# Kernel tuning notes

Measured on AMD Instinct MI355X. Metric: run time of the kernel, lower is better.

Reference implementation:

```python
import jax, jax.numpy as jnp
import numpy as np

BIAS_VALUE = -1e30


def apply_rope(inputs, positions, max_wavelength=10000):
    # inputs: [B, T, H, Dh]; positions: [B, T]
    head_dim = inputs.shape[-1]
    fraction = 2 * jnp.arange(0, head_dim // 2) / head_dim
    timescale = max_wavelength ** fraction
    sinusoid_inp = positions[..., jnp.newaxis] / timescale[jnp.newaxis, :]  # [B, T, Dh/2]
    sinusoid_inp = sinusoid_inp[..., jnp.newaxis, :]                        # [B, T, 1, Dh/2]
    sin = jnp.sin(sinusoid_inp)
    cos = jnp.cos(sinusoid_inp)
    first_half, second_half = jnp.split(inputs, 2, axis=-1)
    first_part = first_half * cos - second_half * sin
    second_part = second_half * cos + first_half * sin
    return jnp.concatenate([first_part, second_part], axis=-1).astype(inputs.dtype)


def rms_norm(x, scale):
    var = jnp.mean(jnp.square(x), axis=-1, keepdims=True)
    return x * jax.lax.rsqrt(var + 1e-6) * (1 + scale)


def setup_inputs() -> dict:
    key = jax.random.key(0)
    ks = jax.random.split(key, 12)
    B, T, D, H, Dh = 4, 2048, 512, 8, 64
    q = jax.random.normal(ks[0], (B, T, D), jnp.float32)
    kv = jax.random.normal(ks[1], (B, T, D), jnp.float32)
    mask = jnp.broadcast_to(jnp.tril(jnp.ones((T, T), bool))[None, None], (B, 1, T, T))
    pos = jnp.broadcast_to(jnp.arange(T, dtype=jnp.int32), (B, T))
    s = 0.02
    return {
        "q": q, "kv": kv, "mask": mask, "q_positions": pos, "kv_positions": pos,
        "wq": jax.random.normal(ks[2], (D, H * Dh), jnp.float32) * s,
        "bq": jnp.zeros((H * Dh,), jnp.float32),
        "wk": jax.random.normal(ks[3], (D, H * Dh), jnp.float32) * s,
        "bk": jnp.zeros((H * Dh,), jnp.float32),
        "wv": jax.random.normal(ks[4], (D, H * Dh), jnp.float32) * s,
        "bv": jnp.zeros((H * Dh,), jnp.float32),
        "scale_q": jax.random.normal(ks[5], (Dh,), jnp.float32) * s,
        "scale_k": jax.random.normal(ks[6], (Dh,), jnp.float32) * s,
        "wo": jax.random.normal(ks[7], (H * Dh, D), jnp.float32) * s,
        "bo": jnp.zeros((D,), jnp.float32),
    }


def reference(q, kv, mask, q_positions, kv_positions,
              wq, bq, wk, bk, wv, bv, scale_q, scale_k, wo, bo):
    B, T, D = q.shape
    H = 8
    Dh = wq.shape[1] // H
    qk_size = Dh

    def proj(x, w, b):
        y = x @ w + b
        return y.reshape(*x.shape[:-1], H, -1)  # [B, T, H, Dh]

    query_heads = rms_norm(proj(q, wq, bq), scale_q)
    key_heads = rms_norm(proj(kv, wk, bk), scale_k)
    value_heads = proj(kv, wv, bv)

    query_heads = apply_rope(query_heads, q_positions)
    key_heads = apply_rope(key_heads, kv_positions)

    attn_logits = jnp.einsum('bthd,bThd->bhtT', query_heads, key_heads)
    attn_logits = attn_logits / np.sqrt(qk_size).astype(q.dtype)
    attn_logits = jnp.where(mask, attn_logits, BIAS_VALUE)
    attn_weights = jax.nn.softmax(attn_logits, axis=-1)
    attn_weights = jnp.where(mask, attn_weights, 0)
    attn = jnp.einsum('bhtT,bThd->bthd', attn_weights, value_heads)
    attn = attn.reshape(B, T, -1)
    return attn @ wo + bo
```

## Files before the change

### kernel.cpp

```cpp
#include <hip/hip_runtime.h>
#include <hip/hip_bf16.h>
#include <cstdint>

#define B_ 4
#define T_ 2048
#define D_ 512
#define H_ 8

typedef __bf16 bf16x8 __attribute__((ext_vector_type(8)));
typedef __bf16 bf16x4 __attribute__((ext_vector_type(4)));
typedef float f32x4 __attribute__((ext_vector_type(4)));

__device__ inline void gload_lds16(const void* g, void* l) {
    __builtin_amdgcn_global_load_lds(
        (const __attribute__((address_space(1))) void*)g,
        (__attribute__((address_space(3))) void*)l, 16, 0, 0);
}

__global__ void cast2_kernel(const float* __restrict__ qf, const float* __restrict__ kvf,
                             __bf16* __restrict__ qb, __bf16* __restrict__ kvb, int n4) {
    int stride = gridDim.x * blockDim.x;
    for (int i = blockIdx.x * blockDim.x + threadIdx.x; i < 2 * n4; i += stride) {
        const float* src = (i < n4) ? qf : kvf;
        __bf16* dst = (i < n4) ? qb : kvb;
        int j = (i < n4) ? i : i - n4;
        float4 v = reinterpret_cast<const float4*>(src)[j];
        bf16x4 o = { (__bf16)v.x, (__bf16)v.y, (__bf16)v.z, (__bf16)v.w };
        reinterpret_cast<bf16x4*>(dst)[j] = o;
    }
}

__global__ void transpose_w4_kernel(const float* __restrict__ wq, const float* __restrict__ wk,
                                    const float* __restrict__ wv, const float* __restrict__ wo,
                                    __bf16* __restrict__ wqkvT, __bf16* __restrict__ woT) {
    __shared__ float tile[32][33];
    int z = blockIdx.z;
    const float* in = (z == 0) ? wq : (z == 1) ? wk : (z == 2) ? wv : wo;
    __bf16* out = (z < 3) ? wqkvT + (size_t)z * D_ * D_ : woT;
    int tx = threadIdx.x & 31, ty = threadIdx.x >> 5;
    int r0 = blockIdx.y * 32, c0 = blockIdx.x * 32;
#pragma unroll
    for (int i = 0; i < 4; i++)
        tile[ty + i * 8][tx] = in[(size_t)(r0 + ty + i * 8) * D_ + c0 + tx];
    __syncthreads();
#pragma unroll
    for (int i = 0; i < 4; i++)
        out[(size_t)(c0 + ty + i * 8) * D_ + r0 + tx] = (__bf16)tile[tx][ty + i * 8];
}

__global__ void rope_table_kernel(float2* __restrict__ tab) {
    int i = blockIdx.x * 256 + threadIdx.x;
    int p = i >> 5, d2 = i & 31;
    float inv_ts = exp2f((float)d2 * (-13.28771237954945f / 32.0f));
    float ang = (float)p * inv_ts;
    float sv, cv;
    __sincosf(ang, &sv, &cv);
    tab[i] = make_float2(cv, sv);
}

template<int MODE>
__global__ __launch_bounds__(256, 2) void gemm_tile_kernel(
    const __bf16* __restrict__ Xq, const __bf16* __restrict__ Xkv,
    const __bf16* __restrict__ WT,
    const float* __restrict__ biasQ, const float* __restrict__ biasK,
    const float* __restrict__ biasV,
    float* __restrict__ outf, __bf16* __restrict__ qh, __bf16* __restrict__ kh,
    __bf16* __restrict__ vt,
    const float* __restrict__ scale_q, const float* __restrict__ scale_k,
    const int* __restrict__ qpos, const int* __restrict__ kpos,
    const float2* __restrict__ rtab, int M, int Ntot, int K) {
    __shared__ __bf16 Ab[2][128 * 32];
    __shared__ __bf16 Bb[2][128 * 32];

    const int tid = threadIdx.x;
    const int lane = tid & 63, widx = tid >> 6;
    const int lo = lane & 15, hi = lane >> 4;
    const int wm = widx >> 1, wn = widx & 1;

    const int nwg = gridDim.x;
    const int q8 = nwg >> 3;
    int bid = blockIdx.x;
    int swz = (bid & 7) * q8 + (bid >> 3);
    const int ntn = Ntot >> 7;
    const int m0 = (swz / ntn) << 7;
    const int nt = swz % ntn;
    const int n0g = nt << 7;
    const int seg = (MODE == 3) ? (nt >> 2) : 0;
    const __bf16* X = (MODE == 3 && seg > 0) ? Xkv : Xq;

    const int srow = tid >> 2;
    const int sslot = tid & 3;

    f32x4 acc[4][4] = {};

    auto stage = [&](int kc, int bufi) {
#pragma unroll
        for (int i = 0; i < 2; i++) {
            int row = i * 64 + srow;
            int cs = sslot ^ ((row >> 1) & 3);
            gload_lds16(X + (size_t)(m0 + row) * K + kc + cs * 8,
                        &Ab[bufi][(i * 64 + widx * 16) * 32]);
        }
#pragma unroll
        for (int i = 0; i < 2; i++) {
            int row = i * 64 + srow;
            int cs = sslot ^ ((row >> 1) & 3);
            gload_lds16(WT + (size_t)(n0g + row) * K + kc + cs * 8,
                        &Bb[bufi][(i * 64 + widx * 16) * 32]);
        }
    };

    const int nks = K >> 5;
    stage(0, 0);
    __syncthreads();
    int cur = 0;

    for (int ks = 0; ks < nks; ks++) {
        if (ks + 1 < nks) stage((ks + 1) << 5, cur ^ 1);

        bf16x8 a[4], bvec[4];
#pragma unroll
        for (int mf = 0; mf < 4; mf++) {
            int R = wm * 64 + mf * 16 + lo;
            a[mf] = *reinterpret_cast<const bf16x8*>(&Ab[cur][R * 32 + ((hi ^ ((R >> 1) & 3)) << 3)]);
        }
#pragma unroll
        for (int nf = 0; nf < 4; nf++) {
            int R = wn * 64 + nf * 16 + lo;
            bvec[nf] = *reinterpret_cast<const bf16x8*>(&Bb[cur][R * 32 + ((hi ^ ((R >> 1) & 3)) << 3)]);
        }
#pragma unroll
        for (int mf = 0; mf < 4; mf++)
#pragma unroll
            for (int nf = 0; nf < 4; nf++)
                acc[mf][nf] = __builtin_amdgcn_mfma_f32_16x16x32_bf16(a[mf], bvec[nf], acc[mf][nf], 0, 0, 0);

        __syncthreads();
        cur ^= 1;
    }

    const int mrow0 = m0 + wm * 64;

    if (MODE == 0) {
        const int ncol0 = n0g + wn * 64;
        float bs[4];
#pragma unroll
        for (int nf = 0; nf < 4; nf++) bs[nf] = biasQ[ncol0 + nf * 16 + lo];
#pragma unroll
        for (int mf = 0; mf < 4; mf++)
#pragma unroll
            for (int nf = 0; nf < 4; nf++)
#pragma unroll
                for (int r = 0; r < 4; r++) {
                    int row = mrow0 + mf * 16 + hi * 4 + r;
                    outf[(size_t)row * Ntot + ncol0 + nf * 16 + lo] = acc[mf][nf][r] + bs[nf];
                }
    } else {
        const int ncol0 = ((nt & 3) << 7) + wn * 64;
        const int h = ncol0 >> 6;
        const float* bias = (seg == 0) ? biasQ : (seg == 1) ? biasK : biasV;
        float bs[4];
#pragma unroll
        for (int nf = 0; nf < 4; nf++) bs[nf] = bias[ncol0 + nf * 16 + lo];

        if (seg < 2) {
            const float* scale = seg ? scale_k : scale_q;
            const int* pos = seg ? kpos : qpos;
            __bf16* dst0 = seg ? kh : qh;
            float sc4[4];
#pragma unroll
            for (int nf = 0; nf < 4; nf++) sc4[nf] = 1.0f + scale[nf * 16 + lo];
#pragma unroll
            for (int mf = 0; mf < 4; mf++) {
#pragma unroll
                for (int r = 0; r < 4; r++) {
                    int row = mrow0 + mf * 16 + hi * 4 + r;
                    float y0 = acc[mf][0][r] + bs[0];
                    float y1 = acc[mf][1][r] + bs[1];
                    float y2 = acc[mf][2][r] + bs[2];
                    float y3 = acc[mf][3][r] + bs[3];
                    float ps = y0 * y0 + y1 * y1 + y2 * y2 + y3 * y3;
#pragma unroll
                    for (int off = 1; off < 16; off <<= 1) ps += __shfl_xor(ps, off);
                    float rmsf = rsqrtf(ps * (1.0f / 64.0f) + 1e-6f);
                    int p = pos[row];
                    float2 c0 = rtab[p * 32 + lo];
                    float2 c1 = rtab[p * 32 + 16 + lo];
                    float z0 = y0 * rmsf * sc4[0];
                    float z1 = y1 * rmsf * sc4[1];
                    float z2 = y2 * rmsf * sc4[2];
                    float z3 = y3 * rmsf * sc4[3];
                    int b = row >> 11, t = row & (T_ - 1);
                    __bf16* dst = dst0 + ((size_t)(b * H_ + h) * T_ + t) * 64;
                    dst[lo]      = (__bf16)(z0 * c0.x - z2 * c0.y);
                    dst[16 + lo] = (__bf16)(z1 * c1.x - z3 * c1.y);
                    dst[32 + lo] = (__bf16)(z2 * c0.x + z0 * c0.y);
                    dst[48 + lo] = (__bf16)(z3 * c1.x + z1 * c1.y);
                }
            }
        } else {
#pragma unroll
            for (int mf = 0; mf < 4; mf++) {
                int row0 = mrow0 + mf * 16 + hi * 4;
                int b = row0 >> 11, t0 = row0 & (T_ - 1);
#pragma unroll
                for (int nf = 0; nf < 4; nf++) {
                    int d = nf * 16 + lo;
                    bf16x4 pk = { (__bf16)(acc[mf][nf][0] + bs[nf]), (__bf16)(acc[mf][nf][1] + bs[nf]),
                                  (__bf16)(acc[mf][nf][2] + bs[nf]), (__bf16)(acc[mf][nf][3] + bs[nf]) };
                    *reinterpret_cast<bf16x4*>(vt + ((size_t)(b * H_ + h) * 64 + d) * T_ + t0) = pk;
                }
            }
        }
    }
}

__global__ __launch_bounds__(256, 3) void attn_kernel(const __bf16* __restrict__ qh,
                                                      const __bf16* __restrict__ kh,
                                                      const __bf16* __restrict__ vt,
                                                      __bf16* __restrict__ attn) {
    __shared__ __bf16 kbuf[2][64 * 64];
    __shared__ __bf16 vbuf[2][64 * 64];
    __shared__ __bf16 plds[4][16][72];

    const int lane = threadIdx.x & 63, widx = threadIdx.x >> 6;
    const int lo = lane & 15, hi = lane >> 4;
    const int bh = blockIdx.x;
    const int sid = 31 - blockIdx.y;
    const int ntiles = sid + 1;
    const int qb = sid * 64 + widx * 16;
    const __bf16* Qg = qh + (size_t)bh * T_ * 64;
    const __bf16* Kg = kh + (size_t)bh * T_ * 64;
    const __bf16* Vg = vt + (size_t)bh * 64 * T_;
    const int b = bh >> 3, h = bh & 7;

    const int srow = lane >> 3;
    const int sslot = lane & 7;
    const int schunk = sslot ^ srow;

    bf16x8 qa[2];
#pragma unroll
    for (int c = 0; c < 2; c++)
        qa[c] = *reinterpret_cast<const bf16x8*>(Qg + (size_t)(qb + lo) * 64 + c * 32 + hi * 8);

    f32x4 o[4] = {};
    float m = -1e30f, l = 0.0f;

    auto stage = [&](int tile, int bufi) {
        const int kvb0 = tile * 64;
#pragma unroll
        for (int i = 0; i < 2; i++) {
            int r = widx * 16 + i * 8 + srow;
            gload_lds16(Kg + (size_t)(kvb0 + r) * 64 + schunk * 8,
                        &kbuf[bufi][(widx * 16 + i * 8) * 64]);
        }
#pragma unroll
        for (int i = 0; i < 2; i++) {
            int r = widx * 16 + i * 8 + srow;
            gload_lds16(Vg + (size_t)r * T_ + kvb0 + schunk * 8,
                        &vbuf[bufi][(widx * 16 + i * 8) * 64]);
        }
    };

    stage(0, 0);
    __syncthreads();
    int cur = 0;

    for (int j = 0; j < ntiles; ++j) {
        if (j + 1 < ntiles) stage(j + 1, cur ^ 1);

        f32x4 s[4] = {};
        __builtin_amdgcn_s_setprio(1);
#pragma unroll
        for (int c = 0; c < 2; c++) {
#pragma unroll
            for (int f = 0; f < 4; f++) {
                int R = f * 16 + lo;
                int C = c * 4 + hi;
                bf16x8 kb = *reinterpret_cast<const bf16x8*>(
                    &kbuf[cur][R * 64 + ((C ^ (lo & 7)) << 3)]);
                s[f] = __builtin_amdgcn_mfma_f32_16x16x32_bf16(kb, qa[c], s[f], 0, 0, 0);
            }
        }
        __builtin_amdgcn_s_setprio(0);

        const bool diag = (j == ntiles - 1);
        float pm = -1e30f;
#pragma unroll
        for (int f = 0; f < 4; f++)
#pragma unroll
            for (int r = 0; r < 4; r++) {
                float v = s[f][r];
                if (diag && (f * 16 + hi * 4 + r > widx * 16 + lo)) v = -1e30f;
                s[f][r] = v;
                pm = fmaxf(pm, v);
            }
        pm = fmaxf(pm, __shfl_xor(pm, 16));
        pm = fmaxf(pm, __shfl_xor(pm, 32));

        if (!__all(pm <= m + 64.0f)) {
            float mn = fmaxf(m, pm);
            float alpha = __expf((m - mn) * 0.125f);
            l *= alpha;
#pragma unroll
            for (int n = 0; n < 4; n++)
#pragma unroll
                for (int r = 0; r < 4; r++) o[n][r] *= alpha;
            m = mn;
        }

        const float negm = -m * 0.125f;
        float ps = 0.0f;
        bf16x4 pk[4];
#pragma unroll
        for (int f = 0; f < 4; f++) {
#pragma unroll
            for (int r = 0; r < 4; r++) {
                float e = __expf(fmaf(s[f][r], 0.125f, negm));
                ps += e;
                pk[f][r] = (__bf16)e;
            }
        }
        ps += __shfl_xor(ps, 16);
        ps += __shfl_xor(ps, 32);
        l += ps;

#pragma unroll
        for (int f = 0; f < 4; f++)
            *reinterpret_cast<bf16x4*>(&plds[widx][lo][f * 16 + hi * 4]) = pk[f];
        bf16x8 pa0 = *reinterpret_cast<const bf16x8*>(&plds[widx][lo][hi * 8]);
        bf16x8 pa1 = *reinterpret_cast<const bf16x8*>(&plds[widx][lo][32 + hi * 8]);

        __builtin_amdgcn_s_setprio(1);
#pragma unroll
        for (int n = 0; n < 4; n++) {
#pragma unroll
            for (int c = 0; c < 2; c++) {
                int R = n * 16 + lo;
                int C = c * 4 + hi;
                bf16x8 vb = *reinterpret_cast<const bf16x8*>(
                    &vbuf[cur][R * 64 + ((C ^ (lo & 7)) << 3)]);
                o[n] = __builtin_amdgcn_mfma_f32_16x16x32_bf16(vb, c ? pa1 : pa0, o[n], 0, 0, 0);
            }
        }
        __builtin_amdgcn_s_setprio(0);

        __syncthreads();
        cur ^= 1;
    }

    const float inv = 1.0f / l;
    const int qrow = qb + lo;
#pragma unroll
    for (int n = 0; n < 4; n++) {
        bf16x4 pk = { (__bf16)(o[n][0] * inv), (__bf16)(o[n][1] * inv),
                      (__bf16)(o[n][2] * inv), (__bf16)(o[n][3] * inv) };
        *reinterpret_cast<bf16x4*>(attn + ((size_t)b * T_ + qrow) * D_ + h * 64 + n * 16 + hi * 4) = pk;
    }
}

extern "C" void kernel_launch(void* const* d_in, const int* in_sizes, int n_in,
                              void* d_out, int out_size, void* d_ws, size_t ws_size,
                              hipStream_t stream) {
    const float* q  = (const float*)d_in[0];
    const float* kv = (const float*)d_in[1];
    const int* qpos = (const int*)d_in[3];
    const int* kpos = (const int*)d_in[4];
    const float* wq = (const float*)d_in[5];
    const float* bq = (const float*)d_in[6];
    const float* wk = (const float*)d_in[7];
    const float* bk = (const float*)d_in[8];
    const float* wv = (const float*)d_in[9];
    const float* bv = (const float*)d_in[10];
    const float* scale_q = (const float*)d_in[11];
    const float* scale_k = (const float*)d_in[12];
    const float* wo = (const float*)d_in[13];
    const float* bo = (const float*)d_in[14];
    float* out = (float*)d_out;

    char* ws = (char*)d_ws;
    size_t off = 0;
    auto alloc = [&](size_t bytes) {
        void* p = ws + off;
        off += (bytes + 255) & ~(size_t)255;
        return p;
    };
    const size_t MD = (size_t)B_ * T_ * D_;
    __bf16* qb16   = (__bf16*)alloc(MD * 2);
    __bf16* kvb16  = (__bf16*)alloc(MD * 2);
    __bf16* wqkvT  = (__bf16*)alloc((size_t)3 * D_ * D_ * 2);
    __bf16* woT    = (__bf16*)alloc((size_t)D_ * D_ * 2);
    __bf16* qh  = (__bf16*)alloc(MD * 2);
    __bf16* kh  = (__bf16*)alloc(MD * 2);
    __bf16* vt  = (__bf16*)alloc(MD * 2);
    float2* rtab = (float2*)alloc((size_t)T_ * 32 * sizeof(float2));
    __bf16* attn = qb16;

    cast2_kernel<<<2048, 256, 0, stream>>>(q, kv, qb16, kvb16, (int)(MD / 4));
    transpose_w4_kernel<<<dim3(16, 16, 4), 256, 0, stream>>>(wq, wk, wv, wo, wqkvT, woT);
    rope_table_kernel<<<(T_ * 32) / 256, 256, 0, stream>>>(rtab);

    const int M = B_ * T_;
    gemm_tile_kernel<3><<<(M / 128) * (3 * D_ / 128), 256, 0, stream>>>(
        qb16, kvb16, wqkvT, bq, bk, bv, nullptr, qh, kh, vt,
        scale_q, scale_k, qpos, kpos, rtab, M, 3 * D_, D_);
    attn_kernel<<<dim3(B_ * H_, 32), 256, 0, stream>>>(qh, kh, vt, attn);
    gemm_tile_kernel<0><<<(M / 128) * (D_ / 128), 256, 0, stream>>>(
        attn, nullptr, woT, bo, nullptr, nullptr, out, nullptr, nullptr, nullptr,
        nullptr, nullptr, nullptr, nullptr, nullptr, M, D_, D_);
}
```

Measured before the change: 96.53 us.

## Double attention query tile per block and fold softmax scale into Q

Each attention block now processes 128 query rows (32 per warp, two 16-row groups) instead of 64, so each staged K/V tile feeds twice as many MFMAs and the grid halves. The softmax scale 1/sqrt(64)*log2(e) is folded into the Q projection epilogue, so the attention loop can use exp2f directly without a per-element multiply. The lazy-rescale threshold is adjusted to match the log2 domain. This raises register use per warp and halves the block count. It also leaves some warps idle on the final diagonal tile, which may reduce occupancy and load balance.

```diff
diff --git a/kernel.cpp b/kernel.cpp
--- a/kernel.cpp
+++ b/kernel.cpp
@@ -10,6 +10,9 @@
 typedef __bf16 bf16x8 __attribute__((ext_vector_type(8)));
 typedef __bf16 bf16x4 __attribute__((ext_vector_type(4)));
 typedef float f32x4 __attribute__((ext_vector_type(4)));
+
+#define QSCALE 0.18033688011112042f
+#define DEFER_THR 11.5415603f
 
 __device__ inline void gload_lds16(const void* g, void* l) {
     __builtin_amdgcn_global_load_lds(
@@ -167,9 +170,10 @@
             const float* scale = seg ? scale_k : scale_q;
             const int* pos = seg ? kpos : qpos;
             __bf16* dst0 = seg ? kh : qh;
+            const float qmul = seg ? 1.0f : QSCALE;
             float sc4[4];
 #pragma unroll
-            for (int nf = 0; nf < 4; nf++) sc4[nf] = 1.0f + scale[nf * 16 + lo];
+            for (int nf = 0; nf < 4; nf++) sc4[nf] = (1.0f + scale[nf * 16 + lo]) * qmul;
 #pragma unroll
             for (int mf = 0; mf < 4; mf++) {
 #pragma unroll
@@ -221,14 +225,14 @@
                                                       __bf16* __restrict__ attn) {
     __shared__ __bf16 kbuf[2][64 * 64];
     __shared__ __bf16 vbuf[2][64 * 64];
-    __shared__ __bf16 plds[4][16][72];
+    __shared__ __bf16 plds[4][32][72];
 
     const int lane = threadIdx.x & 63, widx = threadIdx.x >> 6;
     const int lo = lane & 15, hi = lane >> 4;
     const int bh = blockIdx.x;
-    const int sid = 31 - blockIdx.y;
-    const int ntiles = sid + 1;
-    const int qb = sid * 64 + widx * 16;
+    const int sid = 15 - blockIdx.y;
+    const int ntiles = 2 * sid + 2;
+    const int qb = sid * 128 + widx * 32;
     const __bf16* Qg = qh + (size_t)bh * T_ * 64;
     const __bf16* Kg = kh + (size_t)bh * T_ * 64;
     const __bf16* Vg = vt + (size_t)bh * 64 * T_;
@@ -238,13 +242,16 @@
     const int sslot = lane & 7;
     const int schunk = sslot ^ srow;
 
-    bf16x8 qa[2];
-#pragma unroll
-    for (int c = 0; c < 2; c++)
-        qa[c] = *reinterpret_cast<const bf16x8*>(Qg + (size_t)(qb + lo) * 64 + c * 32 + hi * 8);
-
-    f32x4 o[4] = {};
-    float m = -1e30f, l = 0.0f;
+    bf16x8 qa[2][2];
+#pragma unroll
+    for (int g = 0; g < 2; g++)
+#pragma unroll
+        for (int c = 0; c < 2; c++)
+            qa[g][c] = *reinterpret_cast<const bf16x8*>(
+                Qg + (size_t)(qb + g * 16 + lo) * 64 + c * 32 + hi * 8);
+
+    f32x4 o[2][4] = {};
+    float m[2] = { -1e30f, -1e30f }, l[2] = { 0.0f, 0.0f };
 
     auto stage = [&](int tile, int bufi) {
         const int kvb0 = tile * 64;
@@ -269,93 +276,118 @@
     for (int j = 0; j < ntiles; ++j) {
         if (j + 1 < ntiles) stage(j + 1, cur ^ 1);
 
-        f32x4 s[4] = {};
-        __builtin_amdgcn_s_setprio(1);
-#pragma unroll
-        for (int c = 0; c < 2; c++) {
-#pragma unroll
-            for (int f = 0; f < 4; f++) {
-                int R = f * 16 + lo;
-                int C = c * 4 + hi;
-                bf16x8 kb = *reinterpret_cast<const bf16x8*>(
-                    &kbuf[cur][R * 64 + ((C ^ (lo & 7)) << 3)]);
-                s[f] = __builtin_amdgcn_mfma_f32_16x16x32_bf16(kb, qa[c], s[f], 0, 0, 0);
-            }
-        }
-        __builtin_amdgcn_s_setprio(0);
-
-        const bool diag = (j == ntiles - 1);
-        float pm = -1e30f;
-#pragma unroll
-        for (int f = 0; f < 4; f++)
-#pragma unroll
-            for (int r = 0; r < 4; r++) {
-                float v = s[f][r];
-                if (diag && (f * 16 + hi * 4 + r > widx * 16 + lo)) v = -1e30f;
-                s[f][r] = v;
-                pm = fmaxf(pm, v);
-            }
-        pm = fmaxf(pm, __shfl_xor(pm, 16));
-        pm = fmaxf(pm, __shfl_xor(pm, 32));
-
-        if (!__all(pm <= m + 64.0f)) {
-            float mn = fmaxf(m, pm);
-            float alpha = __expf((m - mn) * 0.125f);
-            l *= alpha;
-#pragma unroll
-            for (int n = 0; n < 4; n++)
-#pragma unroll
-                for (int r = 0; r < 4; r++) o[n][r] *= alpha;
-            m = mn;
-        }
-
-        const float negm = -m * 0.125f;
-        float ps = 0.0f;
-        bf16x4 pk[4];
-#pragma unroll
-        for (int f = 0; f < 4; f++) {
-#pragma unroll
-            for (int r = 0; r < 4; r++) {
-                float e = __expf(fmaf(s[f][r], 0.125f, negm));
-                ps += e;
-                pk[f][r] = (__bf16)e;
-            }
-        }
-        ps += __shfl_xor(ps, 16);
-        ps += __shfl_xor(ps, 32);
-        l += ps;
-
-#pragma unroll
-        for (int f = 0; f < 4; f++)
-            *reinterpret_cast<bf16x4*>(&plds[widx][lo][f * 16 + hi * 4]) = pk[f];
-        bf16x8 pa0 = *reinterpret_cast<const bf16x8*>(&plds[widx][lo][hi * 8]);
-        bf16x8 pa1 = *reinterpret_cast<const bf16x8*>(&plds[widx][lo][32 + hi * 8]);
-
-        __builtin_amdgcn_s_setprio(1);
-#pragma unroll
-        for (int n = 0; n < 4; n++) {
+        const int dj = j - 2 * sid;
+        const bool active = !(dj == 1 && widx < 2);
+        if (active) {
+            f32x4 s[2][4] = {};
+            __builtin_amdgcn_s_setprio(1);
 #pragma unroll
             for (int c = 0; c < 2; c++) {
-                int R = n * 16 + lo;
-                int C = c * 4 + hi;
-                bf16x8 vb = *reinterpret_cast<const bf16x8*>(
-                    &vbuf[cur][R * 64 + ((C ^ (lo & 7)) << 3)]);
-                o[n] = __builtin_amdgcn_mfma_f32_16x16x32_bf16(vb, c ? pa1 : pa0, o[n], 0, 0, 0);
-            }
-        }
-        __builtin_amdgcn_s_setprio(0);
+#pragma unroll
+                for (int f = 0; f < 4; f++) {
+                    int R = f * 16 + lo;
+                    int C = c * 4 + hi;
+                    bf16x8 kb = *reinterpret_cast<const bf16x8*>(
+                        &kbuf[cur][R * 64 + ((C ^ (lo & 7)) << 3)]);
+                    s[0][f] = __builtin_amdgcn_mfma_f32_16x16x32_bf16(kb, qa[0][c], s[0][f], 0, 0, 0);
+                    s[1][f] = __builtin_amdgcn_mfma_f32_16x16x32_bf16(kb, qa[1][c], s[1][f], 0, 0, 0);
+                }
+            }
+            __builtin_amdgcn_s_setprio(0);
+
+            const bool diag = (dj == 0 && widx < 2) || (dj == 1 && widx >= 2);
+            float pm[2] = { -1e30f, -1e30f };
+#pragma unroll
+            for (int g = 0; g < 2; g++)
+#pragma unroll
+                for (int f = 0; f < 4; f++)
+#pragma unroll
+                    for (int r = 0; r < 4; r++) {
+                        float v = s[g][f][r];
+                        if (diag && (j * 64 + f * 16 + hi * 4 + r > qb + g * 16 + lo)) v = -1e30f;
+                        s[g][f][r] = v;
+                        pm[g] = fmaxf(pm[g], v);
+                    }
+#pragma unroll
+            for (int g = 0; g < 2; g++) {
+                pm[g] = fmaxf(pm[g], __shfl_xor(pm[g], 16));
+                pm[g] = fmaxf(pm[g], __shfl_xor(pm[g], 32));
+            }
+
+            if (!__all(fmaxf(pm[0] - m[0], pm[1] - m[1]) <= DEFER_THR)) {
+#pragma unroll
+                for (int g = 0; g < 2; g++) {
+                    float mn = fmaxf(m[g], pm[g]);
+                    float alpha = exp2f(m[g] - mn);
+                    l[g] *= alpha;
+#pragma unroll
+                    for (int n = 0; n < 4; n++)
+#pragma unroll
+                        for (int r = 0; r < 4; r++) o[g][n][r] *= alpha;
+                    m[g] = mn;
+                }
+            }
+
+            bf16x4 pk[2][4];
+#pragma unroll
+            for (int g = 0; g < 2; g++) {
+                float ps = 0.0f;
+#pragma unroll
+                for (int f = 0; f < 4; f++)
+#pragma unroll
+                    for (int r = 0; r < 4; r++) {
+                        float e = exp2f(s[g][f][r] - m[g]);
+                        ps += e;
+                        pk[g][f][r] = (__bf16)e;
+                    }
+                ps += __shfl_xor(ps, 16);
+                ps += __shfl_xor(ps, 32);
+                l[g] += ps;
+            }
+
+#pragma unroll
+            for (int g = 0; g < 2; g++)
+#pragma unroll
+                for (int f = 0; f < 4; f++)
+                    *reinterpret_cast<bf16x4*>(&plds[widx][g * 16 + lo][f * 16 + hi * 4]) = pk[g][f];
+            bf16x8 pa[2][2];
+#pragma unroll
+            for (int g = 0; g < 2; g++)
+#pragma unroll
+                for (int c = 0; c < 2; c++)
+                    pa[g][c] = *reinterpret_cast<const bf16x8*>(
+                        &plds[widx][g * 16 + lo][c * 32 + hi * 8]);
+
+            __builtin_amdgcn_s_setprio(1);
+#pragma unroll
+            for (int n = 0; n < 4; n++) {
+#pragma unroll
+                for (int c = 0; c < 2; c++) {
+                    int R = n * 16 + lo;
+                    int C = c * 4 + hi;
+                    bf16x8 vb = *reinterpret_cast<const bf16x8*>(
+                        &vbuf[cur][R * 64 + ((C ^ (lo & 7)) << 3)]);
+                    o[0][n] = __builtin_amdgcn_mfma_f32_16x16x32_bf16(vb, pa[0][c], o[0][n], 0, 0, 0);
+                    o[1][n] = __builtin_amdgcn_mfma_f32_16x16x32_bf16(vb, pa[1][c], o[1][n], 0, 0, 0);
+                }
+            }
+            __builtin_amdgcn_s_setprio(0);
+        }
 
         __syncthreads();
         cur ^= 1;
     }
 
-    const float inv = 1.0f / l;
-    const int qrow = qb + lo;
-#pragma unroll
-    for (int n = 0; n < 4; n++) {
-        bf16x4 pk = { (__bf16)(o[n][0] * inv), (__bf16)(o[n][1] * inv),
-                      (__bf16)(o[n][2] * inv), (__bf16)(o[n][3] * inv) };
-        *reinterpret_cast<bf16x4*>(attn + ((size_t)b * T_ + qrow) * D_ + h * 64 + n * 16 + hi * 4) = pk;
+#pragma unroll
+    for (int g = 0; g < 2; g++) {
+        const float inv = 1.0f / l[g];
+        const int qrow = qb + g * 16 + lo;
+#pragma unroll
+        for (int n = 0; n < 4; n++) {
+            bf16x4 pk = { (__bf16)(o[g][n][0] * inv), (__bf16)(o[g][n][1] * inv),
+                          (__bf16)(o[g][n][2] * inv), (__bf16)(o[g][n][3] * inv) };
+            *reinterpret_cast<bf16x4*>(attn + ((size_t)b * T_ + qrow) * D_ + h * 64 + n * 16 + hi * 4) = pk;
+        }
     }
 }
 
@@ -404,7 +436,7 @@
     gemm_tile_kernel<3><<<(M / 128) * (3 * D_ / 128), 256, 0, stream>>>(
         qb16, kvb16, wqkvT, bq, bk, bv, nullptr, qh, kh, vt,
         scale_q, scale_k, qpos, kpos, rtab, M, 3 * D_, D_);
-    attn_kernel<<<dim3(B_ * H_, 32), 256, 0, stream>>>(qh, kh, vt, attn);
+    attn_kernel<<<dim3(B_ * H_, 16), 256, 0, stream>>>(qh, kh, vt, attn);
     gemm_tile_kernel<0><<<(M / 128) * (D_ / 128), 256, 0, stream>>>(
         attn, nullptr, woT, bo, nullptr, nullptr, out, nullptr, nullptr, nullptr,
         nullptr, nullptr, nullptr, nullptr, nullptr, M, D_, D_);
```

New measurement: 122.7 us. +27.1%, slower.

## Use 128-row query blocks with 8 waves and fold softmax scale into Q

Applied to the files above, without the earlier changes.

The attention kernel now processes 128 query rows per block with 512 threads (8 waves), so each K/V tile staged in LDS is shared by twice as many query rows and each thread issues one load per tile instead of two. The last tile is skipped by the first four waves, whose rows are fully masked there. The 1/sqrt(d)*log2(e) factor is folded into the Q projection epilogue so the softmax uses exp2 without a per-element multiply, and the deferred-rescale threshold is adjusted to match. Costs are fewer blocks (less parallelism and coarser causal load balance), some idle waves on the diagonal tile, and Q rounded to bf16 after scaling.

```diff
diff --git a/kernel.cpp b/kernel.cpp
--- a/kernel.cpp
+++ b/kernel.cpp
@@ -10,6 +10,9 @@
 typedef __bf16 bf16x8 __attribute__((ext_vector_type(8)));
 typedef __bf16 bf16x4 __attribute__((ext_vector_type(4)));
 typedef float f32x4 __attribute__((ext_vector_type(4)));
+
+#define QSCALE 0.18033688011112042f
+#define DEFER_THR 11.5415603f
 
 __device__ inline void gload_lds16(const void* g, void* l) {
     __builtin_amdgcn_global_load_lds(
@@ -167,9 +170,10 @@
             const float* scale = seg ? scale_k : scale_q;
             const int* pos = seg ? kpos : qpos;
             __bf16* dst0 = seg ? kh : qh;
+            const float qmul = seg ? 1.0f : QSCALE;
             float sc4[4];
 #pragma unroll
-            for (int nf = 0; nf < 4; nf++) sc4[nf] = 1.0f + scale[nf * 16 + lo];
+            for (int nf = 0; nf < 4; nf++) sc4[nf] = (1.0f + scale[nf * 16 + lo]) * qmul;
 #pragma unroll
             for (int mf = 0; mf < 4; mf++) {
 #pragma unroll
@@ -215,28 +219,27 @@
     }
 }
 
-__global__ __launch_bounds__(256, 3) void attn_kernel(const __bf16* __restrict__ qh,
+__global__ __launch_bounds__(512, 6) void attn_kernel(const __bf16* __restrict__ qh,
                                                       const __bf16* __restrict__ kh,
                                                       const __bf16* __restrict__ vt,
                                                       __bf16* __restrict__ attn) {
     __shared__ __bf16 kbuf[2][64 * 64];
     __shared__ __bf16 vbuf[2][64 * 64];
-    __shared__ __bf16 plds[4][16][72];
+    __shared__ __bf16 plds[8][16][72];
 
     const int lane = threadIdx.x & 63, widx = threadIdx.x >> 6;
     const int lo = lane & 15, hi = lane >> 4;
     const int bh = blockIdx.x;
-    const int sid = 31 - blockIdx.y;
-    const int ntiles = sid + 1;
-    const int qb = sid * 64 + widx * 16;
+    const int sid = 15 - blockIdx.y;
+    const int ntiles = 2 * sid + 2;
+    const int qb = sid * 128 + widx * 16;
     const __bf16* Qg = qh + (size_t)bh * T_ * 64;
     const __bf16* Kg = kh + (size_t)bh * T_ * 64;
     const __bf16* Vg = vt + (size_t)bh * 64 * T_;
     const int b = bh >> 3, h = bh & 7;
 
-    const int srow = lane >> 3;
-    const int sslot = lane & 7;
-    const int schunk = sslot ^ srow;
+    const int srow = widx * 8 + (lane >> 3);
+    const int schunk = (lane & 7) ^ (srow & 7);
 
     bf16x8 qa[2];
 #pragma unroll
@@ -248,18 +251,10 @@
 
     auto stage = [&](int tile, int bufi) {
         const int kvb0 = tile * 64;
-#pragma unroll
-        for (int i = 0; i < 2; i++) {
-            int r = widx * 16 + i * 8 + srow;
-            gload_lds16(Kg + (size_t)(kvb0 + r) * 64 + schunk * 8,
-                        &kbuf[bufi][(widx * 16 + i * 8) * 64]);
-        }
-#pragma unroll
-        for (int i = 0; i < 2; i++) {
-            int r = widx * 16 + i * 8 + srow;
-            gload_lds16(Vg + (size_t)r * T_ + kvb0 + schunk * 8,
-                        &vbuf[bufi][(widx * 16 + i * 8) * 64]);
-        }
+        gload_lds16(Kg + (size_t)(kvb0 + srow) * 64 + schunk * 8,
+                    &kbuf[bufi][widx * 8 * 64]);
+        gload_lds16(Vg + (size_t)srow * T_ + kvb0 + schunk * 8,
+                    &vbuf[bufi][widx * 8 * 64]);
     };
 
     stage(0, 0);
@@ -269,81 +264,84 @@
     for (int j = 0; j < ntiles; ++j) {
         if (j + 1 < ntiles) stage(j + 1, cur ^ 1);
 
-        f32x4 s[4] = {};
-        __builtin_amdgcn_s_setprio(1);
-#pragma unroll
-        for (int c = 0; c < 2; c++) {
+        const int dj = j - 2 * sid;
+        const bool active = !(dj == 1 && widx < 4);
+        if (active) {
+            f32x4 s[4] = {};
+            __builtin_amdgcn_s_setprio(1);
+#pragma unroll
+            for (int c = 0; c < 2; c++) {
+#pragma unroll
+                for (int f = 0; f < 4; f++) {
+                    int R = f * 16 + lo;
+                    int C = c * 4 + hi;
+                    bf16x8 kb = *reinterpret_cast<const bf16x8*>(
+                        &kbuf[cur][R * 64 + ((C ^ (lo & 7)) << 3)]);
+                    s[f] = __builtin_amdgcn_mfma_f32_16x16x32_bf16(kb, qa[c], s[f], 0, 0, 0);
+                }
+            }
+            __builtin_amdgcn_s_setprio(0);
+
+            const bool diag = (dj == 0 && widx < 4) || (dj == 1 && widx >= 4);
+            float pm = -1e30f;
+#pragma unroll
+            for (int f = 0; f < 4; f++)
+#pragma unroll
+                for (int r = 0; r < 4; r++) {
+                    float v = s[f][r];
+                    if (diag && (j * 64 + f * 16 + hi * 4 + r > qb + lo)) v = -1e30f;
+                    s[f][r] = v;
+                    pm = fmaxf(pm, v);
+                }
+            pm = fmaxf(pm, __shfl_xor(pm, 16));
+            pm = fmaxf(pm, __shfl_xor(pm, 32));
+
+            if (!__all(pm <= m + DEFER_THR)) {
+                float mn = fmaxf(m, pm);
+                float alpha = exp2f(m - mn);
+                l *= alpha;
+#pragma unroll
+                for (int n = 0; n < 4; n++)
+#pragma unroll
+                    for (int r = 0; r < 4; r++) o[n][r] *= alpha;
+                m = mn;
+            }
+
+            float ps = 0.0f;
+            bf16x4 pk[4];
 #pragma unroll
             for (int f = 0; f < 4; f++) {
-                int R = f * 16 + lo;
-                int C = c * 4 + hi;
-                bf16x8 kb = *reinterpret_cast<const bf16x8*>(
-                    &kbuf[cur][R * 64 + ((C ^ (lo & 7)) << 3)]);
-                s[f] = __builtin_amdgcn_mfma_f32_16x16x32_bf16(kb, qa[c], s[f], 0, 0, 0);
-            }
-        }
-        __builtin_amdgcn_s_setprio(0);
-
-        const bool diag = (j == ntiles - 1);
-        float pm = -1e30f;
-#pragma unroll
-        for (int f = 0; f < 4; f++)
-#pragma unroll
-            for (int r = 0; r < 4; r++) {
-                float v = s[f][r];
-                if (diag && (f * 16 + hi * 4 + r > widx * 16 + lo)) v = -1e30f;
-                s[f][r] = v;
-                pm = fmaxf(pm, v);
-            }
-        pm = fmaxf(pm, __shfl_xor(pm, 16));
-        pm = fmaxf(pm, __shfl_xor(pm, 32));
-
-        if (!__all(pm <= m + 64.0f)) {
-            float mn = fmaxf(m, pm);
-            float alpha = __expf((m - mn) * 0.125f);
-            l *= alpha;
-#pragma unroll
-            for (int n = 0; n < 4; n++)
-#pragma unroll
-                for (int r = 0; r < 4; r++) o[n][r] *= alpha;
-            m = mn;
-        }
-
-        const float negm = -m * 0.125f;
-        float ps = 0.0f;
-        bf16x4 pk[4];
-#pragma unroll
-        for (int f = 0; f < 4; f++) {
-#pragma unroll
-            for (int r = 0; r < 4; r++) {
-                float e = __expf(fmaf(s[f][r], 0.125f, negm));
-                ps += e;
-                pk[f][r] = (__bf16)e;
-            }
-        }
-        ps += __shfl_xor(ps, 16);
-        ps += __shfl_xor(ps, 32);
-        l += ps;
-
-#pragma unroll
-        for (int f = 0; f < 4; f++)
-            *reinterpret_cast<bf16x4*>(&plds[widx][lo][f * 16 + hi * 4]) = pk[f];
-        bf16x8 pa0 = *reinterpret_cast<const bf16x8*>(&plds[widx][lo][hi * 8]);
-        bf16x8 pa1 = *reinterpret_cast<const bf16x8*>(&plds[widx][lo][32 + hi * 8]);
-
-        __builtin_amdgcn_s_setprio(1);
-#pragma unroll
-        for (int n = 0; n < 4; n++) {
-#pragma unroll
-            for (int c = 0; c < 2; c++) {
-                int R = n * 16 + lo;
-                int C = c * 4 + hi;
-                bf16x8 vb = *reinterpret_cast<const bf16x8*>(
-                    &vbuf[cur][R * 64 + ((C ^ (lo & 7)) << 3)]);
-                o[n] = __builtin_amdgcn_mfma_f32_16x16x32_bf16(vb, c ? pa1 : pa0, o[n], 0, 0, 0);
-            }
-        }
-        __builtin_amdgcn_s_setprio(0);
+#pragma unroll
+                for (int r = 0; r < 4; r++) {
+                    float e = exp2f(s[f][r] - m);
+                    ps += e;
+                    pk[f][r] = (__bf16)e;
+                }
+            }
+            ps += __shfl_xor(ps, 16);
+            ps += __shfl_xor(ps, 32);
+            l += ps;
+
+#pragma unroll
+            for (int f = 0; f < 4; f++)
+                *reinterpret_cast<bf16x4*>(&plds[widx][lo][f * 16 + hi * 4]) = pk[f];
+            bf16x8 pa0 = *reinterpret_cast<const bf16x8*>(&plds[widx][lo][hi * 8]);
+            bf16x8 pa1 = *reinterpret_cast<const bf16x8*>(&plds[widx][lo][32 + hi * 8]);
+
+            __builtin_amdgcn_s_setprio(1);
+#pragma unroll
+            for (int n = 0; n < 4; n++) {
+#pragma unroll
+                for (int c = 0; c < 2; c++) {
+                    int R = n * 16 + lo;
+                    int C = c * 4 + hi;
+                    bf16x8 vb = *reinterpret_cast<const bf16x8*>(
+                        &vbuf[cur][R * 64 + ((C ^ (lo & 7)) << 3)]);
+                    o[n] = __builtin_amdgcn_mfma_f32_16x16x32_bf16(vb, c ? pa1 : pa0, o[n], 0, 0, 0);
+                }
+            }
+            __builtin_amdgcn_s_setprio(0);
+        }
 
         __syncthreads();
         cur ^= 1;
@@ -353,9 +351,9 @@
     const int qrow = qb + lo;
 #pragma unroll
     for (int n = 0; n < 4; n++) {
-        bf16x4 pk = { (__bf16)(o[n][0] * inv), (__bf16)(o[n][1] * inv),
-                      (__bf16)(o[n][2] * inv), (__bf16)(o[n][3] * inv) };
-        *reinterpret_cast<bf16x4*>(attn + ((size_t)b * T_ + qrow) * D_ + h * 64 + n * 16 + hi * 4) = pk;
+        bf16x4 pko = { (__bf16)(o[n][0] * inv), (__bf16)(o[n][1] * inv),
+                       (__bf16)(o[n][2] * inv), (__bf16)(o[n][3] * inv) };
+        *reinterpret_cast<bf16x4*>(attn + ((size_t)b * T_ + qrow) * D_ + h * 64 + n * 16 + hi * 4) = pko;
     }
 }
 
@@ -404,7 +402,7 @@
     gemm_tile_kernel<3><<<(M / 128) * (3 * D_ / 128), 256, 0, stream>>>(
         qb16, kvb16, wqkvT, bq, bk, bv, nullptr, qh, kh, vt,
         scale_q, scale_k, qpos, kpos, rtab, M, 3 * D_, D_);
-    attn_kernel<<<dim3(B_ * H_, 32), 256, 0, stream>>>(qh, kh, vt, attn);
+    attn_kernel<<<dim3(B_ * H_, 16), 512, 0, stream>>>(qh, kh, vt, attn);
     gemm_tile_kernel<0><<<(M / 128) * (D_ / 128), 256, 0, stream>>>(
         attn, nullptr, woT, bo, nullptr, nullptr, out, nullptr, nullptr, nullptr,
         nullptr, nullptr, nullptr, nullptr, nullptr, M, D_, D_);
```

Measured after the change: 110.4 us. 1.14x slower.

## Fold softmax scale into Q and use fixed max shift instead of online max

Applied to the files above, without the earlier changes.

The 1/sqrt(d)·log2(e) factor is folded into the Q RMS-norm scale in the projection epilogue. The attention loop then drops the running-max computation, its cross-lane shuffles and the rescaling of the output accumulators. A constant shift of -16 is preloaded into the MFMA accumulator so each logit becomes a single exp2. This relies on QK-norm bounding the logits, so it risks overflow or underflow if scale_q or scale_k were large.

```diff
diff --git a/kernel.cpp b/kernel.cpp
--- a/kernel.cpp
+++ b/kernel.cpp
@@ -10,6 +10,9 @@
 typedef __bf16 bf16x8 __attribute__((ext_vector_type(8)));
 typedef __bf16 bf16x4 __attribute__((ext_vector_type(4)));
 typedef float f32x4 __attribute__((ext_vector_type(4)));
+
+#define QSCALE 0.18033688011112042f
+#define MSHIFT 16.0f
 
 __device__ inline void gload_lds16(const void* g, void* l) {
     __builtin_amdgcn_global_load_lds(
@@ -167,9 +170,10 @@
             const float* scale = seg ? scale_k : scale_q;
             const int* pos = seg ? kpos : qpos;
             __bf16* dst0 = seg ? kh : qh;
+            const float qmul = seg ? 1.0f : QSCALE;
             float sc4[4];
 #pragma unroll
-            for (int nf = 0; nf < 4; nf++) sc4[nf] = 1.0f + scale[nf * 16 + lo];
+            for (int nf = 0; nf < 4; nf++) sc4[nf] = (1.0f + scale[nf * 16 + lo]) * qmul;
 #pragma unroll
             for (int mf = 0; mf < 4; mf++) {
 #pragma unroll
@@ -244,7 +248,8 @@
         qa[c] = *reinterpret_cast<const bf16x8*>(Qg + (size_t)(qb + lo) * 64 + c * 32 + hi * 8);
 
     f32x4 o[4] = {};
-    float m = -1e30f, l = 0.0f;
+    float l = 0.0f;
+    const f32x4 minit = { -MSHIFT, -MSHIFT, -MSHIFT, -MSHIFT };
 
     auto stage = [&](int tile, int bufi) {
         const int kvb0 = tile * 64;
@@ -269,7 +274,7 @@
     for (int j = 0; j < ntiles; ++j) {
         if (j + 1 < ntiles) stage(j + 1, cur ^ 1);
 
-        f32x4 s[4] = {};
+        f32x4 s[4] = { minit, minit, minit, minit };
         __builtin_amdgcn_s_setprio(1);
 #pragma unroll
         for (int c = 0; c < 2; c++) {
@@ -284,39 +289,21 @@
         }
         __builtin_amdgcn_s_setprio(0);
 
-        const bool diag = (j == ntiles - 1);
-        float pm = -1e30f;
-#pragma unroll
-        for (int f = 0; f < 4; f++)
-#pragma unroll
-            for (int r = 0; r < 4; r++) {
-                float v = s[f][r];
-                if (diag && (f * 16 + hi * 4 + r > widx * 16 + lo)) v = -1e30f;
-                s[f][r] = v;
-                pm = fmaxf(pm, v);
-            }
-        pm = fmaxf(pm, __shfl_xor(pm, 16));
-        pm = fmaxf(pm, __shfl_xor(pm, 32));
-
-        if (!__all(pm <= m + 64.0f)) {
-            float mn = fmaxf(m, pm);
-            float alpha = __expf((m - mn) * 0.125f);
-            l *= alpha;
-#pragma unroll
-            for (int n = 0; n < 4; n++)
-#pragma unroll
-                for (int r = 0; r < 4; r++) o[n][r] *= alpha;
-            m = mn;
-        }
-
-        const float negm = -m * 0.125f;
+        if (j == ntiles - 1) {
+#pragma unroll
+            for (int f = 0; f < 4; f++)
+#pragma unroll
+                for (int r = 0; r < 4; r++)
+                    if (f * 16 + hi * 4 + r > widx * 16 + lo) s[f][r] = -1e30f;
+        }
+
         float ps = 0.0f;
         bf16x4 pk[4];
 #pragma unroll
         for (int f = 0; f < 4; f++) {
 #pragma unroll
             for (int r = 0; r < 4; r++) {
-                float e = __expf(fmaf(s[f][r], 0.125f, negm));
+                float e = __builtin_amdgcn_exp2f(s[f][r]);
                 ps += e;
                 pk[f][r] = (__bf16)e;
             }
@@ -353,9 +340,9 @@
     const int qrow = qb + lo;
 #pragma unroll
     for (int n = 0; n < 4; n++) {
-        bf16x4 pk = { (__bf16)(o[n][0] * inv), (__bf16)(o[n][1] * inv),
-                      (__bf16)(o[n][2] * inv), (__bf16)(o[n][3] * inv) };
-        *reinterpret_cast<bf16x4*>(attn + ((size_t)b * T_ + qrow) * D_ + h * 64 + n * 16 + hi * 4) = pk;
+        bf16x4 pko = { (__bf16)(o[n][0] * inv), (__bf16)(o[n][1] * inv),
+                       (__bf16)(o[n][2] * inv), (__bf16)(o[n][3] * inv) };
+        *reinterpret_cast<bf16x4*>(attn + ((size_t)b * T_ + qrow) * D_ + h * 64 + n * 16 + hi * 4) = pko;
     }
 }
 
```

After: 89.36 us. 1.08x faster.
